# Kernel tuning notes

Measured on AMD Instinct MI355X. Metric: run time of the kernel, lower is better.

The kernel has to match this reference:

```python
import jax, jax.numpy as jnp
import numpy as np

R = 16                      # grid resolution per axis -> R**3 = 4096 experts
E = R ** 3
L_XYZ = 10                  # xyz positional-encoding frequencies -> input_ch = 63
L_DIR = 4                   # dir positional-encoding frequencies -> input_ch_views = 27
HID = 32                    # KiloNeRF W
AABB_MIN = -1.5
AABB_MAX = 1.5


def posenc(x, L):
    # NeRF positional encoding: [x, sin(2^l x), cos(2^l x)] for l in 0..L-1
    freqs = 2.0 ** jnp.arange(L, dtype=x.dtype)          # (L,)
    xb = x[..., None, :] * freqs[:, None]                # (..., L, 3)
    enc = jnp.concatenate([jnp.sin(xb), jnp.cos(xb)], axis=-1)  # (..., L, 6)
    return jnp.concatenate([x, enc.reshape(x.shape[:-1] + (-1,))], axis=-1)


def _linear_init(key, shape, fan_in):
    s = 1.0 / np.sqrt(fan_in)
    return jax.random.uniform(key, shape, jnp.float32, -s, s)


def setup_inputs() -> dict:
    key = jax.random.key(0)
    ks = jax.random.split(key, 16)
    in_pts = 3 + 6 * L_XYZ     # 63
    in_dirs = 3 + 6 * L_DIR    # 27
    in_view = in_dirs + HID    # 59
    return {
        "pts": jax.random.normal(ks[0], (1024, 64, 3), jnp.float32),
        "viewdirs": jax.random.normal(ks[1], (1024, 3), jnp.float32),
        "W1": _linear_init(ks[2], (E, in_pts, HID), in_pts),
        "b1": _linear_init(ks[3], (E, HID), in_pts),
        "W2": _linear_init(ks[4], (E, HID, HID), HID),
        "b2": _linear_init(ks[5], (E, HID), HID),
        "Wf": _linear_init(ks[6], (E, HID, HID), HID),
        "bf": _linear_init(ks[7], (E, HID), HID),
        "Wsig": _linear_init(ks[8], (E, HID, 1), HID),
        "bsig": _linear_init(ks[9], (E, 1), HID),
        "Wv": _linear_init(ks[10], (E, in_view, HID), in_view),
        "bv": _linear_init(ks[11], (E, HID), in_view),
        "Wrgb": _linear_init(ks[12], (E, HID, 3), HID),
        "brgb": _linear_init(ks[13], (E, 3), HID),
    }


def reference(pts, viewdirs, W1, b1, W2, b2, Wf, bf, Wsig, bsig, Wv, bv, Wrgb, brgb):
    N_rays, N_samples, _ = pts.shape
    p = pts.reshape(-1, 3)                                           # (N,3)
    d = jnp.broadcast_to(viewdirs[:, None, :], (N_rays, N_samples, 3)).reshape(-1, 3)

    # voxel index per point (Network._get_index)
    norm = (p - AABB_MIN) / (AABB_MAX - AABB_MIN)
    scaled = jnp.clip(norm * R, 0.0, R - 1.0)
    idx = scaled.astype(jnp.int32)                                   # (N,3)
    e = idx[:, 0] * (R * R) + idx[:, 1] * R + idx[:, 2]              # (N,) expert id

    xp = posenc(p, L_XYZ)                                            # (N,63)
    xd = posenc(d, L_DIR)                                            # (N,27)

    # grouped tiny-MLP dispatch, vectorized as per-point gathered weights
    h = jax.nn.relu(jnp.einsum('ni,nio->no', xp, W1[e]) + b1[e])     # (N,32)
    h = jax.nn.relu(jnp.einsum('ni,nio->no', h, W2[e]) + b2[e])      # (N,32)
    sigma = jnp.einsum('ni,nio->no', h, Wsig[e]) + bsig[e]           # (N,1)
    feat = jnp.einsum('ni,nio->no', h, Wf[e]) + bf[e]                # (N,32)
    hv = jnp.concatenate([feat, xd], axis=-1)                        # (N,59)
    hv = jax.nn.relu(jnp.einsum('ni,nio->no', hv, Wv[e]) + bv[e])    # (N,32)
    rgb = jnp.einsum('ni,nio->no', hv, Wrgb[e]) + brgb[e]            # (N,3)

    return rgb.reshape(N_rays, N_samples, 3), sigma.reshape(N_rays, N_samples, 1)
```

## Files before the change

### kernel.cpp

```cpp
#include <hip/hip_runtime.h>


#define CAP 256

#define WS_COUNTS 0
#define WS_OFFSETS 4096
#define WS_CURSOR 8192
#define WS_ORDER 12288

#define L_W1 0
#define L_W2 2016
#define L_WF 3040
#define L_WV 4064
#define L_WS 5952
#define L_WR 5984
#define L_B1 6080
#define L_B2 6112
#define L_BF 6144
#define L_BV 6176
#define L_BSR 6208
#define L_TOT 6212

__device__ __forceinline__ int expert_id(float px, float py, float pz) {
    float nx = (px - (-1.5f)) / 3.0f;
    float ny = (py - (-1.5f)) / 3.0f;
    float nz = (pz - (-1.5f)) / 3.0f;
    float sx = fminf(fmaxf(nx * 16.0f, 0.0f), 15.0f);
    float sy = fminf(fmaxf(ny * 16.0f, 0.0f), 15.0f);
    float sz = fminf(fmaxf(nz * 16.0f, 0.0f), 15.0f);
    return (int)sx * 256 + (int)sy * 16 + (int)sz;
}

__device__ __forceinline__ void gl16(const float* __restrict__ src, float* dst,
                                     int lane) {
    __builtin_amdgcn_global_load_lds(
        (const __attribute__((address_space(1))) unsigned int*)(src + 4 * lane),
        (__attribute__((address_space(3))) unsigned int*)(dst + 4 * lane),
        16, 0, 0);
}

__device__ __forceinline__ void stage_lds(const float* __restrict__ src,
                                          float* dst, int nfl, int lane) {
    int c = 0;
    for (; c + 256 <= nfl; c += 256) gl16(src + c, dst + c, lane);
    const int rem = nfl - c;
    if (4 * lane < rem) gl16(src + c, dst + c, lane);
}

__device__ __forceinline__ float enc_val(int idx, float x, float y, float z) {
    if (idx < 3) return (idx == 0) ? x : ((idx == 1) ? y : z);
    const int k = idx - 3;
    const int l = k / 6;
    const int r = k - 6 * l;
    const int c = (r < 3) ? r : r - 3;
    const float cv = (c == 0) ? x : ((c == 1) ? y : z);
    const float a = ldexpf(cv, l);
    return (r < 3) ? sinf(a) : cosf(a);
}

__global__ __launch_bounds__(256) void scatter_cap_kernel(
    const float* __restrict__ pts, int* __restrict__ counts,
    int* __restrict__ order, int n) {
    const int i = blockIdx.x * 256 + threadIdx.x;
    if (i < n) {
        const int e = expert_id(pts[3 * i + 0], pts[3 * i + 1], pts[3 * i + 2]);
        const int r = atomicAdd(&counts[e], 1);
        if (r < CAP) order[e * CAP + r] = i;
    }
}

__global__ __launch_bounds__(256) void hist_kernel(const float* __restrict__ pts,
                                                   int* __restrict__ counts, int n) {
    int i = blockIdx.x * 256 + threadIdx.x;
    if (i < n) {
        int e = expert_id(pts[3 * i + 0], pts[3 * i + 1], pts[3 * i + 2]);
        atomicAdd(&counts[e], 1);
    }
}

__global__ __launch_bounds__(256) void scan_kernel(const int* __restrict__ counts,
                                                   int* __restrict__ offsets,
                                                   int* __restrict__ cursor) {
    const int tid = threadIdx.x;
    const int lane = tid & 63, wave = tid >> 6;
    const int base = tid * 16;
    int c[16], loc[16], sum = 0;
#pragma unroll
    for (int j = 0; j < 16; ++j) c[j] = counts[base + j];
#pragma unroll
    for (int j = 0; j < 16; ++j) { loc[j] = sum; sum += c[j]; }
    int v = sum;
#pragma unroll
    for (int off = 1; off <= 32; off <<= 1) {
        int u = __shfl_up(v, off, 64);
        if (lane >= off) v += u;
    }
    __shared__ int wtot[4];
    if (lane == 63) wtot[wave] = v;
    __syncthreads();
    int wbase = 0;
    for (int w = 0; w < wave; ++w) wbase += wtot[w];
    const int excl = wbase + v - sum;
#pragma unroll
    for (int j = 0; j < 16; ++j) {
        int o = excl + loc[j];
        offsets[base + j] = o;
        cursor[base + j] = o;
    }
}

__global__ __launch_bounds__(256) void scatter_kernel(const float* __restrict__ pts,
                                                      int* __restrict__ cursor,
                                                      int* __restrict__ order, int n) {
    int i = blockIdx.x * 256 + threadIdx.x;
    if (i < n) {
        int e = expert_id(pts[3 * i + 0], pts[3 * i + 1], pts[3 * i + 2]);
        int pos = atomicAdd(&cursor[e], 1);
        order[pos] = i;
    }
}

__global__ __launch_bounds__(256) void expert_mlp_kernel(
    const float* __restrict__ pts, const float* __restrict__ viewdirs,
    const float* __restrict__ W1, const float* __restrict__ b1,
    const float* __restrict__ W2, const float* __restrict__ b2,
    const float* __restrict__ Wf, const float* __restrict__ bfc,
    const float* __restrict__ Wsig, const float* __restrict__ bsig,
    const float* __restrict__ Wv, const float* __restrict__ bv,
    const float* __restrict__ Wrgb, const float* __restrict__ brgb,
    const int* __restrict__ counts, const int* __restrict__ offsets,
    const int* __restrict__ order,
    float* __restrict__ out_rgb, float* __restrict__ out_sigma,
    int samples, int cap) {

    const int e = blockIdx.x;
    int cnt = counts[e];
    if (cnt == 0) return;
    if (cap > 0 && cnt > cap) cnt = cap;
    const int start = (cap > 0) ? e * cap : offsets[e];
    const int tid = threadIdx.x;
    const int wave = tid >> 6;
    const int lane = tid & 63;
    const int h = lane >> 5;
    const int o = lane & 31;

    __shared__ float lw[L_TOT];
    __shared__ float xs[4][8][64];
    __shared__ float xd[4][8][32];

    if (wave == 0) {
        stage_lds(W1 + (size_t)e * 2016, lw + L_W1, 2016, lane);
    } else if (wave == 1) {
        stage_lds(Wv + (size_t)e * 1888, lw + L_WV, 1888, lane);
    } else if (wave == 2) {
        stage_lds(W2 + (size_t)e * 1024, lw + L_W2, 1024, lane);
        stage_lds(Wsig + (size_t)e * 32, lw + L_WS, 32, lane);
        stage_lds(b1 + (size_t)e * 32, lw + L_B1, 32, lane);
        stage_lds(b2 + (size_t)e * 32, lw + L_B2, 32, lane);
    } else {
        stage_lds(Wf + (size_t)e * 1024, lw + L_WF, 1024, lane);
        stage_lds(Wrgb + (size_t)e * 96, lw + L_WR, 96, lane);
        stage_lds(bfc + (size_t)e * 32, lw + L_BF, 32, lane);
        stage_lds(bv + (size_t)e * 32, lw + L_BV, 32, lane);
    }
    if (tid == 0) lw[L_BSR] = bsig[e];
    if (tid < 3) lw[L_BSR + 1 + tid] = brgb[3 * e + tid];
    __syncthreads();

    const float b1o = lw[L_B1 + o];
    const float b2o = lw[L_B2 + o];
    const float bfo = lw[L_BF + o];
    const float bvo = lw[L_BV + o];
    const float wsg = lw[L_WS + o];
    const float wr0 = lw[L_WR + 3 * o + 0];
    const float wr1 = lw[L_WR + 3 * o + 1];
    const float wr2 = lw[L_WR + 3 * o + 2];
    const float bsg = lw[L_BSR];
    const float br0 = lw[L_BSR + 1], br1 = lw[L_BSR + 2], br2 = lw[L_BSR + 3];

    float* xsA = xs[wave][h];     float* xsB = xs[wave][2 + h];
    float* xsC = xs[wave][4 + h]; float* xsD = xs[wave][6 + h];
    float* xdA = xd[wave][h];     float* xdB = xd[wave][2 + h];
    float* xdC = xd[wave][4 + h]; float* xdD = xd[wave][6 + h];

    const bool pow2 = (samples & (samples - 1)) == 0;
    const int sh = 31 - __clz(samples);

    for (int s0 = 8 * wave; s0 < cnt; s0 += 32) {
        const int sA = s0 + h, sB = s0 + 2 + h, sC = s0 + 4 + h, sD = s0 + 6 + h;
        const bool lA = (sA < cnt), lB = (sB < cnt), lC = (sC < cnt), lD = (sD < cnt);
        const int ptA = order[start + (lA ? sA : cnt - 1)];
        const int ptB = order[start + (lB ? sB : cnt - 1)];
        const int ptC = order[start + (lC ? sC : cnt - 1)];
        const int ptD = order[start + (lD ? sD : cnt - 1)];

        const float pxA = pts[3 * ptA], pyA = pts[3 * ptA + 1], pzA = pts[3 * ptA + 2];
        const float pxB = pts[3 * ptB], pyB = pts[3 * ptB + 1], pzB = pts[3 * ptB + 2];
        const float pxC = pts[3 * ptC], pyC = pts[3 * ptC + 1], pzC = pts[3 * ptC + 2];
        const float pxD = pts[3 * ptD], pyD = pts[3 * ptD + 1], pzD = pts[3 * ptD + 2];
        const int rayA = pow2 ? (ptA >> sh) : (ptA / samples);
        const int rayB = pow2 ? (ptB >> sh) : (ptB / samples);
        const int rayC = pow2 ? (ptC >> sh) : (ptC / samples);
        const int rayD = pow2 ? (ptD >> sh) : (ptD / samples);
        const float dxA = viewdirs[3 * rayA], dyA = viewdirs[3 * rayA + 1], dzA = viewdirs[3 * rayA + 2];
        const float dxB = viewdirs[3 * rayB], dyB = viewdirs[3 * rayB + 1], dzB = viewdirs[3 * rayB + 2];
        const float dxC = viewdirs[3 * rayC], dyC = viewdirs[3 * rayC + 1], dzC = viewdirs[3 * rayC + 2];
        const float dxD = viewdirs[3 * rayD], dyD = viewdirs[3 * rayD + 1], dzD = viewdirs[3 * rayD + 2];

        xsA[o] = enc_val(o, pxA, pyA, pzA);
        xsB[o] = enc_val(o, pxB, pyB, pzB);
        xsC[o] = enc_val(o, pxC, pyC, pzC);
        xsD[o] = enc_val(o, pxD, pyD, pzD);
        if (o < 31) {
            xsA[o + 32] = enc_val(o + 32, pxA, pyA, pzA);
            xsB[o + 32] = enc_val(o + 32, pxB, pyB, pzB);
            xsC[o + 32] = enc_val(o + 32, pxC, pyC, pzC);
            xsD[o + 32] = enc_val(o + 32, pxD, pyD, pzD);
        }
        if (o < 27) {
            xdA[o] = enc_val(o, dxA, dyA, dzA);
            xdB[o] = enc_val(o, dxB, dyB, dzB);
            xdC[o] = enc_val(o, dxC, dyC, dzC);
            xdD[o] = enc_val(o, dxD, dyD, dzD);
        }

        float aA = b1o, aB = b1o, aC = b1o, aD = b1o;
#pragma unroll
        for (int q = 0; q < 15; ++q) {
            const float w0 = lw[L_W1 + (4 * q + 0) * 32 + o];
            const float w1 = lw[L_W1 + (4 * q + 1) * 32 + o];
            const float w2 = lw[L_W1 + (4 * q + 2) * 32 + o];
            const float w3 = lw[L_W1 + (4 * q + 3) * 32 + o];
            const float4 xA = *(const float4*)&xsA[4 * q];
            const float4 xB = *(const float4*)&xsB[4 * q];
            const float4 xC = *(const float4*)&xsC[4 * q];
            const float4 xD = *(const float4*)&xsD[4 * q];
            aA = fmaf(xA.x, w0, aA); aB = fmaf(xB.x, w0, aB);
            aC = fmaf(xC.x, w0, aC); aD = fmaf(xD.x, w0, aD);
            aA = fmaf(xA.y, w1, aA); aB = fmaf(xB.y, w1, aB);
            aC = fmaf(xC.y, w1, aC); aD = fmaf(xD.y, w1, aD);
            aA = fmaf(xA.z, w2, aA); aB = fmaf(xB.z, w2, aB);
            aC = fmaf(xC.z, w2, aC); aD = fmaf(xD.z, w2, aD);
            aA = fmaf(xA.w, w3, aA); aB = fmaf(xB.w, w3, aB);
            aC = fmaf(xC.w, w3, aC); aD = fmaf(xD.w, w3, aD);
        }
#pragma unroll
        for (int i = 60; i < 63; ++i) {
            const float w = lw[L_W1 + i * 32 + o];
            aA = fmaf(xsA[i], w, aA); aB = fmaf(xsB[i], w, aB);
            aC = fmaf(xsC[i], w, aC); aD = fmaf(xsD[i], w, aD);
        }
        xsA[o] = fmaxf(aA, 0.f);  xsB[o] = fmaxf(aB, 0.f);
        xsC[o] = fmaxf(aC, 0.f);  xsD[o] = fmaxf(aD, 0.f);

        aA = b2o; aB = b2o; aC = b2o; aD = b2o;
#pragma unroll
        for (int q = 0; q < 8; ++q) {
            const float w0 = lw[L_W2 + (4 * q + 0) * 32 + o];
            const float w1 = lw[L_W2 + (4 * q + 1) * 32 + o];
            const float w2 = lw[L_W2 + (4 * q + 2) * 32 + o];
            const float w3 = lw[L_W2 + (4 * q + 3) * 32 + o];
            const float4 xA = *(const float4*)&xsA[4 * q];
            const float4 xB = *(const float4*)&xsB[4 * q];
            const float4 xC = *(const float4*)&xsC[4 * q];
            const float4 xD = *(const float4*)&xsD[4 * q];
            aA = fmaf(xA.x, w0, aA); aB = fmaf(xB.x, w0, aB);
            aC = fmaf(xC.x, w0, aC); aD = fmaf(xD.x, w0, aD);
            aA = fmaf(xA.y, w1, aA); aB = fmaf(xB.y, w1, aB);
            aC = fmaf(xC.y, w1, aC); aD = fmaf(xD.y, w1, aD);
            aA = fmaf(xA.z, w2, aA); aB = fmaf(xB.z, w2, aB);
            aC = fmaf(xC.z, w2, aC); aD = fmaf(xD.z, w2, aD);
            aA = fmaf(xA.w, w3, aA); aB = fmaf(xB.w, w3, aB);
            aC = fmaf(xC.w, w3, aC); aD = fmaf(xD.w, w3, aD);
        }
        const float gA = fmaxf(aA, 0.f), gB = fmaxf(aB, 0.f);
        const float gC = fmaxf(aC, 0.f), gD = fmaxf(aD, 0.f);

        {
            float sA2 = gA * wsg, sB2 = gB * wsg, sC2 = gC * wsg, sD2 = gD * wsg;
#pragma unroll
            for (int m = 1; m <= 16; m <<= 1) {
                sA2 += __shfl_xor(sA2, m, 64);
                sB2 += __shfl_xor(sB2, m, 64);
                sC2 += __shfl_xor(sC2, m, 64);
                sD2 += __shfl_xor(sD2, m, 64);
            }
            if (o == 0) {
                if (lA) out_sigma[ptA] = sA2 + bsg;
                if (lB) out_sigma[ptB] = sB2 + bsg;
                if (lC) out_sigma[ptC] = sC2 + bsg;
                if (lD) out_sigma[ptD] = sD2 + bsg;
            }
        }
        xsA[o] = gA; xsB[o] = gB; xsC[o] = gC; xsD[o] = gD;

        aA = bfo; aB = bfo; aC = bfo; aD = bfo;
#pragma unroll
        for (int q = 0; q < 8; ++q) {
            const float w0 = lw[L_WF + (4 * q + 0) * 32 + o];
            const float w1 = lw[L_WF + (4 * q + 1) * 32 + o];
            const float w2 = lw[L_WF + (4 * q + 2) * 32 + o];
            const float w3 = lw[L_WF + (4 * q + 3) * 32 + o];
            const float4 xA = *(const float4*)&xsA[4 * q];
            const float4 xB = *(const float4*)&xsB[4 * q];
            const float4 xC = *(const float4*)&xsC[4 * q];
            const float4 xD = *(const float4*)&xsD[4 * q];
            aA = fmaf(xA.x, w0, aA); aB = fmaf(xB.x, w0, aB);
            aC = fmaf(xC.x, w0, aC); aD = fmaf(xD.x, w0, aD);
            aA = fmaf(xA.y, w1, aA); aB = fmaf(xB.y, w1, aB);
            aC = fmaf(xC.y, w1, aC); aD = fmaf(xD.y, w1, aD);
            aA = fmaf(xA.z, w2, aA); aB = fmaf(xB.z, w2, aB);
            aC = fmaf(xC.z, w2, aC); aD = fmaf(xD.z, w2, aD);
            aA = fmaf(xA.w, w3, aA); aB = fmaf(xB.w, w3, aB);
            aC = fmaf(xC.w, w3, aC); aD = fmaf(xD.w, w3, aD);
        }
        xsA[o] = aA; xsB[o] = aB; xsC[o] = aC; xsD[o] = aD;

        float vA = bvo, vB = bvo, vC = bvo, vD = bvo;
#pragma unroll
        for (int q = 0; q < 8; ++q) {
            const float w0 = lw[L_WV + (4 * q + 0) * 32 + o];
            const float w1 = lw[L_WV + (4 * q + 1) * 32 + o];
            const float w2 = lw[L_WV + (4 * q + 2) * 32 + o];
            const float w3 = lw[L_WV + (4 * q + 3) * 32 + o];
            const float4 xA = *(const float4*)&xsA[4 * q];
            const float4 xB = *(const float4*)&xsB[4 * q];
            const float4 xC = *(const float4*)&xsC[4 * q];
            const float4 xD = *(const float4*)&xsD[4 * q];
            vA = fmaf(xA.x, w0, vA); vB = fmaf(xB.x, w0, vB);
            vC = fmaf(xC.x, w0, vC); vD = fmaf(xD.x, w0, vD);
            vA = fmaf(xA.y, w1, vA); vB = fmaf(xB.y, w1, vB);
            vC = fmaf(xC.y, w1, vC); vD = fmaf(xD.y, w1, vD);
            vA = fmaf(xA.z, w2, vA); vB = fmaf(xB.z, w2, vB);
            vC = fmaf(xC.z, w2, vC); vD = fmaf(xD.z, w2, vD);
            vA = fmaf(xA.w, w3, vA); vB = fmaf(xB.w, w3, vB);
            vC = fmaf(xC.w, w3, vC); vD = fmaf(xD.w, w3, vD);
        }
#pragma unroll
        for (int q = 0; q < 6; ++q) {
            const float w0 = lw[L_WV + (32 + 4 * q + 0) * 32 + o];
            const float w1 = lw[L_WV + (32 + 4 * q + 1) * 32 + o];
            const float w2 = lw[L_WV + (32 + 4 * q + 2) * 32 + o];
            const float w3 = lw[L_WV + (32 + 4 * q + 3) * 32 + o];
            const float4 xA = *(const float4*)&xdA[4 * q];
            const float4 xB = *(const float4*)&xdB[4 * q];
            const float4 xC = *(const float4*)&xdC[4 * q];
            const float4 xD = *(const float4*)&xdD[4 * q];
            vA = fmaf(xA.x, w0, vA); vB = fmaf(xB.x, w0, vB);
            vC = fmaf(xC.x, w0, vC); vD = fmaf(xD.x, w0, vD);
            vA = fmaf(xA.y, w1, vA); vB = fmaf(xB.y, w1, vB);
            vC = fmaf(xC.y, w1, vC); vD = fmaf(xD.y, w1, vD);
            vA = fmaf(xA.z, w2, vA); vB = fmaf(xB.z, w2, vB);
            vC = fmaf(xC.z, w2, vC); vD = fmaf(xD.z, w2, vD);
            vA = fmaf(xA.w, w3, vA); vB = fmaf(xB.w, w3, vB);
            vC = fmaf(xC.w, w3, vC); vD = fmaf(xD.w, w3, vD);
        }
#pragma unroll
        for (int i = 24; i < 27; ++i) {
            const float w = lw[L_WV + (32 + i) * 32 + o];
            vA = fmaf(xdA[i], w, vA); vB = fmaf(xdB[i], w, vB);
            vC = fmaf(xdC[i], w, vC); vD = fmaf(xdD[i], w, vD);
        }
        const float hA = fmaxf(vA, 0.f), hB = fmaxf(vB, 0.f);
        const float hC = fmaxf(vC, 0.f), hD = fmaxf(vD, 0.f);

        {
            float r0A = hA * wr0, r1A = hA * wr1, r2A = hA * wr2;
            float r0B = hB * wr0, r1B = hB * wr1, r2B = hB * wr2;
            float r0C = hC * wr0, r1C = hC * wr1, r2C = hC * wr2;
            float r0D = hD * wr0, r1D = hD * wr1, r2D = hD * wr2;
#pragma unroll
            for (int m = 1; m <= 16; m <<= 1) {
                r0A += __shfl_xor(r0A, m, 64); r1A += __shfl_xor(r1A, m, 64); r2A += __shfl_xor(r2A, m, 64);
                r0B += __shfl_xor(r0B, m, 64); r1B += __shfl_xor(r1B, m, 64); r2B += __shfl_xor(r2B, m, 64);
                r0C += __shfl_xor(r0C, m, 64); r1C += __shfl_xor(r1C, m, 64); r2C += __shfl_xor(r2C, m, 64);
                r0D += __shfl_xor(r0D, m, 64); r1D += __shfl_xor(r1D, m, 64); r2D += __shfl_xor(r2D, m, 64);
            }
            if (o == 0) {
                if (lA) { out_rgb[3 * ptA] = r0A + br0; out_rgb[3 * ptA + 1] = r1A + br1; out_rgb[3 * ptA + 2] = r2A + br2; }
                if (lB) { out_rgb[3 * ptB] = r0B + br0; out_rgb[3 * ptB + 1] = r1B + br1; out_rgb[3 * ptB + 2] = r2B + br2; }
                if (lC) { out_rgb[3 * ptC] = r0C + br0; out_rgb[3 * ptC + 1] = r1C + br1; out_rgb[3 * ptC + 2] = r2C + br2; }
                if (lD) { out_rgb[3 * ptD] = r0D + br0; out_rgb[3 * ptD + 1] = r1D + br1; out_rgb[3 * ptD + 2] = r2D + br2; }
            }
        }
    }
}

extern "C" void kernel_launch(void* const* d_in, const int* in_sizes, int n_in,
                              void* d_out, int out_size, void* d_ws, size_t ws_size,
                              hipStream_t stream) {
    const float* pts      = (const float*)d_in[0];
    const float* viewdirs = (const float*)d_in[1];
    const float* W1   = (const float*)d_in[2];
    const float* b1   = (const float*)d_in[3];
    const float* W2   = (const float*)d_in[4];
    const float* b2   = (const float*)d_in[5];
    const float* Wf   = (const float*)d_in[6];
    const float* bfc  = (const float*)d_in[7];
    const float* Wsig = (const float*)d_in[8];
    const float* bsig = (const float*)d_in[9];
    const float* Wv   = (const float*)d_in[10];
    const float* bv   = (const float*)d_in[11];
    const float* Wrgb = (const float*)d_in[12];
    const float* brgb = (const float*)d_in[13];

    const int n = in_sizes[0] / 3;
    const int n_rays = in_sizes[1] / 3;
    const int samples = n / n_rays;

    float* out_rgb = (float*)d_out;
    float* out_sigma = out_rgb + (size_t)n * 3;

    int* ws = (int*)d_ws;
    int* counts = ws + WS_COUNTS;
    int* offsets = ws + WS_OFFSETS;
    int* cursor = ws + WS_CURSOR;
    int* order = ws + WS_ORDER;

    const size_t need_cap = ((size_t)WS_ORDER + (size_t)4096 * CAP) * sizeof(int);
    if (ws_size >= need_cap) {
        hipMemsetAsync(counts, 0, 4096 * sizeof(int), stream);
        scatter_cap_kernel<<<(n + 255) / 256, 256, 0, stream>>>(pts, counts, order, n);
        expert_mlp_kernel<<<4096, 256, 0, stream>>>(
            pts, viewdirs, W1, b1, W2, b2, Wf, bfc, Wsig, bsig, Wv, bv, Wrgb, brgb,
            counts, offsets, order, out_rgb, out_sigma, samples, CAP);
    } else {
        hipMemsetAsync(counts, 0, 4096 * sizeof(int), stream);
        hist_kernel<<<(n + 255) / 256, 256, 0, stream>>>(pts, counts, n);
        scan_kernel<<<1, 256, 0, stream>>>(counts, offsets, cursor);
        scatter_kernel<<<(n + 255) / 256, 256, 0, stream>>>(pts, cursor, order, n);
        expert_mlp_kernel<<<4096, 256, 0, stream>>>(
            pts, viewdirs, W1, b1, W2, b2, Wf, bfc, Wsig, bsig, Wv, bv, Wrgb, brgb,
            counts, offsets, order, out_rgb, out_sigma, samples, 0);
    }
}
```

Before: 210.5 us.

## Process four experts per block with a dedicated producer wave double-buffering weights

Each block now handles up to four consecutive non-empty experts instead of one. A fifth wave acts as a producer that stages the next expert's weight slab into a second LDS buffer while the four compute waves work on the current expert. The goal is to hide weight-load latency and cut per-block launch and setup overhead. In exchange, the grid is four times smaller, LDS use roughly doubles (which may reduce occupancy), and a single wave now does all the staging with block-wide syncs between experts.

```diff
diff --git a/kernel.cpp b/kernel.cpp
--- a/kernel.cpp
+++ b/kernel.cpp
@@ -19,7 +19,7 @@
 #define L_BF 6144
 #define L_BV 6176
 #define L_BSR 6208
-#define L_TOT 6212
+#define SLABF 6224
 
 __device__ __forceinline__ int expert_id(float px, float py, float pz) {
     float nx = (px - (-1.5f)) / 3.0f;
@@ -45,6 +45,28 @@
     for (; c + 256 <= nfl; c += 256) gl16(src + c, dst + c, lane);
     const int rem = nfl - c;
     if (4 * lane < rem) gl16(src + c, dst + c, lane);
+}
+
+__device__ __forceinline__ void stage_slab(
+    float* dst, int e, int lane,
+    const float* __restrict__ W1, const float* __restrict__ W2,
+    const float* __restrict__ Wf, const float* __restrict__ Wv,
+    const float* __restrict__ Wsig, const float* __restrict__ Wrgb,
+    const float* __restrict__ b1, const float* __restrict__ b2,
+    const float* __restrict__ bfc, const float* __restrict__ bv,
+    const float* __restrict__ bsig, const float* __restrict__ brgb) {
+    stage_lds(W1 + (size_t)e * 2016, dst + L_W1, 2016, lane);
+    stage_lds(Wv + (size_t)e * 1888, dst + L_WV, 1888, lane);
+    stage_lds(W2 + (size_t)e * 1024, dst + L_W2, 1024, lane);
+    stage_lds(Wf + (size_t)e * 1024, dst + L_WF, 1024, lane);
+    stage_lds(Wsig + (size_t)e * 32, dst + L_WS, 32, lane);
+    stage_lds(Wrgb + (size_t)e * 96, dst + L_WR, 96, lane);
+    stage_lds(b1 + (size_t)e * 32, dst + L_B1, 32, lane);
+    stage_lds(b2 + (size_t)e * 32, dst + L_B2, 32, lane);
+    stage_lds(bfc + (size_t)e * 32, dst + L_BF, 32, lane);
+    stage_lds(bv + (size_t)e * 32, dst + L_BV, 32, lane);
+    if (lane == 0) dst[L_BSR] = bsig[e];
+    if (lane < 3) dst[L_BSR + 1 + lane] = brgb[3 * e + lane];
 }
 
 __device__ __forceinline__ float enc_val(int idx, float x, float y, float z) {
@@ -120,7 +142,7 @@
     }
 }
 
-__global__ __launch_bounds__(256) void expert_mlp_kernel(
+__global__ __launch_bounds__(320) void expert_mlp_kernel(
     const float* __restrict__ pts, const float* __restrict__ viewdirs,
     const float* __restrict__ W1, const float* __restrict__ b1,
     const float* __restrict__ W2, const float* __restrict__ b2,
@@ -133,256 +155,265 @@
     float* __restrict__ out_rgb, float* __restrict__ out_sigma,
     int samples, int cap) {
 
-    const int e = blockIdx.x;
-    int cnt = counts[e];
-    if (cnt == 0) return;
-    if (cap > 0 && cnt > cap) cnt = cap;
-    const int start = (cap > 0) ? e * cap : offsets[e];
     const int tid = threadIdx.x;
-    const int wave = tid >> 6;
+    const int wv = tid >> 6;
     const int lane = tid & 63;
-    const int h = lane >> 5;
-    const int o = lane & 31;
-
-    __shared__ float lw[L_TOT];
+
+    unsigned pack = 0;
+    int K = 0;
+#pragma unroll
+    for (int j = 0; j < 4; ++j) {
+        if (counts[4 * blockIdx.x + j] > 0) { pack |= (unsigned)j << (8 * K); ++K; }
+    }
+    if (K == 0) return;
+
+    __shared__ float lw[2 * SLABF];
     __shared__ float xs[4][8][64];
     __shared__ float xd[4][8][32];
 
-    if (wave == 0) {
-        stage_lds(W1 + (size_t)e * 2016, lw + L_W1, 2016, lane);
-    } else if (wave == 1) {
-        stage_lds(Wv + (size_t)e * 1888, lw + L_WV, 1888, lane);
-    } else if (wave == 2) {
-        stage_lds(W2 + (size_t)e * 1024, lw + L_W2, 1024, lane);
-        stage_lds(Wsig + (size_t)e * 32, lw + L_WS, 32, lane);
-        stage_lds(b1 + (size_t)e * 32, lw + L_B1, 32, lane);
-        stage_lds(b2 + (size_t)e * 32, lw + L_B2, 32, lane);
-    } else {
-        stage_lds(Wf + (size_t)e * 1024, lw + L_WF, 1024, lane);
-        stage_lds(Wrgb + (size_t)e * 96, lw + L_WR, 96, lane);
-        stage_lds(bfc + (size_t)e * 32, lw + L_BF, 32, lane);
-        stage_lds(bv + (size_t)e * 32, lw + L_BV, 32, lane);
-    }
-    if (tid == 0) lw[L_BSR] = bsig[e];
-    if (tid < 3) lw[L_BSR + 1 + tid] = brgb[3 * e + tid];
-    __syncthreads();
-
-    const float b1o = lw[L_B1 + o];
-    const float b2o = lw[L_B2 + o];
-    const float bfo = lw[L_BF + o];
-    const float bvo = lw[L_BV + o];
-    const float wsg = lw[L_WS + o];
-    const float wr0 = lw[L_WR + 3 * o + 0];
-    const float wr1 = lw[L_WR + 3 * o + 1];
-    const float wr2 = lw[L_WR + 3 * o + 2];
-    const float bsg = lw[L_BSR];
-    const float br0 = lw[L_BSR + 1], br1 = lw[L_BSR + 2], br2 = lw[L_BSR + 3];
-
-    float* xsA = xs[wave][h];     float* xsB = xs[wave][2 + h];
-    float* xsC = xs[wave][4 + h]; float* xsD = xs[wave][6 + h];
-    float* xdA = xd[wave][h];     float* xdB = xd[wave][2 + h];
-    float* xdC = xd[wave][4 + h]; float* xdD = xd[wave][6 + h];
-
     const bool pow2 = (samples & (samples - 1)) == 0;
     const int sh = 31 - __clz(samples);
 
-    for (int s0 = 8 * wave; s0 < cnt; s0 += 32) {
-        const int sA = s0 + h, sB = s0 + 2 + h, sC = s0 + 4 + h, sD = s0 + 6 + h;
-        const bool lA = (sA < cnt), lB = (sB < cnt), lC = (sC < cnt), lD = (sD < cnt);
-        const int ptA = order[start + (lA ? sA : cnt - 1)];
-        const int ptB = order[start + (lB ? sB : cnt - 1)];
-        const int ptC = order[start + (lC ? sC : cnt - 1)];
-        const int ptD = order[start + (lD ? sD : cnt - 1)];
-
-        const float pxA = pts[3 * ptA], pyA = pts[3 * ptA + 1], pzA = pts[3 * ptA + 2];
-        const float pxB = pts[3 * ptB], pyB = pts[3 * ptB + 1], pzB = pts[3 * ptB + 2];
-        const float pxC = pts[3 * ptC], pyC = pts[3 * ptC + 1], pzC = pts[3 * ptC + 2];
-        const float pxD = pts[3 * ptD], pyD = pts[3 * ptD + 1], pzD = pts[3 * ptD + 2];
-        const int rayA = pow2 ? (ptA >> sh) : (ptA / samples);
-        const int rayB = pow2 ? (ptB >> sh) : (ptB / samples);
-        const int rayC = pow2 ? (ptC >> sh) : (ptC / samples);
-        const int rayD = pow2 ? (ptD >> sh) : (ptD / samples);
-        const float dxA = viewdirs[3 * rayA], dyA = viewdirs[3 * rayA + 1], dzA = viewdirs[3 * rayA + 2];
-        const float dxB = viewdirs[3 * rayB], dyB = viewdirs[3 * rayB + 1], dzB = viewdirs[3 * rayB + 2];
-        const float dxC = viewdirs[3 * rayC], dyC = viewdirs[3 * rayC + 1], dzC = viewdirs[3 * rayC + 2];
-        const float dxD = viewdirs[3 * rayD], dyD = viewdirs[3 * rayD + 1], dzD = viewdirs[3 * rayD + 2];
-
-        xsA[o] = enc_val(o, pxA, pyA, pzA);
-        xsB[o] = enc_val(o, pxB, pyB, pzB);
-        xsC[o] = enc_val(o, pxC, pyC, pzC);
-        xsD[o] = enc_val(o, pxD, pyD, pzD);
-        if (o < 31) {
-            xsA[o + 32] = enc_val(o + 32, pxA, pyA, pzA);
-            xsB[o + 32] = enc_val(o + 32, pxB, pyB, pzB);
-            xsC[o + 32] = enc_val(o + 32, pxC, pyC, pzC);
-            xsD[o + 32] = enc_val(o + 32, pxD, pyD, pzD);
-        }
-        if (o < 27) {
-            xdA[o] = enc_val(o, dxA, dyA, dzA);
-            xdB[o] = enc_val(o, dxB, dyB, dzB);
-            xdC[o] = enc_val(o, dxC, dyC, dzC);
-            xdD[o] = enc_val(o, dxD, dyD, dzD);
-        }
-
-        float aA = b1o, aB = b1o, aC = b1o, aD = b1o;
-#pragma unroll
-        for (int q = 0; q < 15; ++q) {
-            const float w0 = lw[L_W1 + (4 * q + 0) * 32 + o];
-            const float w1 = lw[L_W1 + (4 * q + 1) * 32 + o];
-            const float w2 = lw[L_W1 + (4 * q + 2) * 32 + o];
-            const float w3 = lw[L_W1 + (4 * q + 3) * 32 + o];
-            const float4 xA = *(const float4*)&xsA[4 * q];
-            const float4 xB = *(const float4*)&xsB[4 * q];
-            const float4 xC = *(const float4*)&xsC[4 * q];
-            const float4 xD = *(const float4*)&xsD[4 * q];
-            aA = fmaf(xA.x, w0, aA); aB = fmaf(xB.x, w0, aB);
-            aC = fmaf(xC.x, w0, aC); aD = fmaf(xD.x, w0, aD);
-            aA = fmaf(xA.y, w1, aA); aB = fmaf(xB.y, w1, aB);
-            aC = fmaf(xC.y, w1, aC); aD = fmaf(xD.y, w1, aD);
-            aA = fmaf(xA.z, w2, aA); aB = fmaf(xB.z, w2, aB);
-            aC = fmaf(xC.z, w2, aC); aD = fmaf(xD.z, w2, aD);
-            aA = fmaf(xA.w, w3, aA); aB = fmaf(xB.w, w3, aB);
-            aC = fmaf(xC.w, w3, aC); aD = fmaf(xD.w, w3, aD);
-        }
-#pragma unroll
-        for (int i = 60; i < 63; ++i) {
-            const float w = lw[L_W1 + i * 32 + o];
-            aA = fmaf(xsA[i], w, aA); aB = fmaf(xsB[i], w, aB);
-            aC = fmaf(xsC[i], w, aC); aD = fmaf(xsD[i], w, aD);
-        }
-        xsA[o] = fmaxf(aA, 0.f);  xsB[o] = fmaxf(aB, 0.f);
-        xsC[o] = fmaxf(aC, 0.f);  xsD[o] = fmaxf(aD, 0.f);
-
-        aA = b2o; aB = b2o; aC = b2o; aD = b2o;
-#pragma unroll
-        for (int q = 0; q < 8; ++q) {
-            const float w0 = lw[L_W2 + (4 * q + 0) * 32 + o];
-            const float w1 = lw[L_W2 + (4 * q + 1) * 32 + o];
-            const float w2 = lw[L_W2 + (4 * q + 2) * 32 + o];
-            const float w3 = lw[L_W2 + (4 * q + 3) * 32 + o];
-            const float4 xA = *(const float4*)&xsA[4 * q];
-            const float4 xB = *(const float4*)&xsB[4 * q];
-            const float4 xC = *(const float4*)&xsC[4 * q];
-            const float4 xD = *(const float4*)&xsD[4 * q];
-            aA = fmaf(xA.x, w0, aA); aB = fmaf(xB.x, w0, aB);
-            aC = fmaf(xC.x, w0, aC); aD = fmaf(xD.x, w0, aD);
-            aA = fmaf(xA.y, w1, aA); aB = fmaf(xB.y, w1, aB);
-            aC = fmaf(xC.y, w1, aC); aD = fmaf(xD.y, w1, aD);
-            aA = fmaf(xA.z, w2, aA); aB = fmaf(xB.z, w2, aB);
-            aC = fmaf(xC.z, w2, aC); aD = fmaf(xD.z, w2, aD);
-            aA = fmaf(xA.w, w3, aA); aB = fmaf(xB.w, w3, aB);
-            aC = fmaf(xC.w, w3, aC); aD = fmaf(xD.w, w3, aD);
-        }
-        const float gA = fmaxf(aA, 0.f), gB = fmaxf(aB, 0.f);
-        const float gC = fmaxf(aC, 0.f), gD = fmaxf(aD, 0.f);
-
-        {
-            float sA2 = gA * wsg, sB2 = gB * wsg, sC2 = gC * wsg, sD2 = gD * wsg;
-#pragma unroll
-            for (int m = 1; m <= 16; m <<= 1) {
-                sA2 += __shfl_xor(sA2, m, 64);
-                sB2 += __shfl_xor(sB2, m, 64);
-                sC2 += __shfl_xor(sC2, m, 64);
-                sD2 += __shfl_xor(sD2, m, 64);
+    if (wv == 4) {
+        const int e0 = 4 * blockIdx.x + (int)(pack & 3u);
+        stage_slab(lw, e0, lane, W1, W2, Wf, Wv, Wsig, Wrgb, b1, b2, bfc, bv,
+                   bsig, brgb);
+    }
+    __syncthreads();
+
+    for (int k = 0; k < K; ++k) {
+        float* lwc = lw + (k & 1) * SLABF;
+        if (wv == 4) {
+            if (k + 1 < K) {
+                const int en = 4 * blockIdx.x + (int)((pack >> (8 * (k + 1))) & 3u);
+                stage_slab(lw + ((k + 1) & 1) * SLABF, en, lane, W1, W2, Wf, Wv,
+                           Wsig, Wrgb, b1, b2, bfc, bv, bsig, brgb);
             }
-            if (o == 0) {
-                if (lA) out_sigma[ptA] = sA2 + bsg;
-                if (lB) out_sigma[ptB] = sB2 + bsg;
-                if (lC) out_sigma[ptC] = sC2 + bsg;
-                if (lD) out_sigma[ptD] = sD2 + bsg;
+        } else {
+            const int e = 4 * blockIdx.x + (int)((pack >> (8 * k)) & 3u);
+            int cnt = counts[e];
+            if (cap > 0 && cnt > cap) cnt = cap;
+            const int start = (cap > 0) ? e * cap : offsets[e];
+            const int wave = wv;
+            const int h = lane >> 5;
+            const int o = lane & 31;
+
+            const float b1o = lwc[L_B1 + o];
+            const float b2o = lwc[L_B2 + o];
+            const float bfo = lwc[L_BF + o];
+            const float bvo = lwc[L_BV + o];
+            const float wsg = lwc[L_WS + o];
+            const float wr0 = lwc[L_WR + 3 * o + 0];
+            const float wr1 = lwc[L_WR + 3 * o + 1];
+            const float wr2 = lwc[L_WR + 3 * o + 2];
+            const float bsg = lwc[L_BSR];
+            const float br0 = lwc[L_BSR + 1], br1 = lwc[L_BSR + 2], br2 = lwc[L_BSR + 3];
+
+            float* xsA = xs[wave][h];     float* xsB = xs[wave][2 + h];
+            float* xsC = xs[wave][4 + h]; float* xsD = xs[wave][6 + h];
+            float* xdA = xd[wave][h];     float* xdB = xd[wave][2 + h];
+            float* xdC = xd[wave][4 + h]; float* xdD = xd[wave][6 + h];
+
+            for (int s0 = 8 * wave; s0 < cnt; s0 += 32) {
+                const int sA = s0 + h, sB = s0 + 2 + h, sC = s0 + 4 + h, sD = s0 + 6 + h;
+                const bool lA = (sA < cnt), lB = (sB < cnt), lC = (sC < cnt), lD = (sD < cnt);
+                const int ptA = order[start + (lA ? sA : cnt - 1)];
+                const int ptB = order[start + (lB ? sB : cnt - 1)];
+                const int ptC = order[start + (lC ? sC : cnt - 1)];
+                const int ptD = order[start + (lD ? sD : cnt - 1)];
+
+                const float pxA = pts[3 * ptA], pyA = pts[3 * ptA + 1], pzA = pts[3 * ptA + 2];
+                const float pxB = pts[3 * ptB], pyB = pts[3 * ptB + 1], pzB = pts[3 * ptB + 2];
+                const float pxC = pts[3 * ptC], pyC = pts[3 * ptC + 1], pzC = pts[3 * ptC + 2];
+                const float pxD = pts[3 * ptD], pyD = pts[3 * ptD + 1], pzD = pts[3 * ptD + 2];
+                const int rayA = pow2 ? (ptA >> sh) : (ptA / samples);
+                const int rayB = pow2 ? (ptB >> sh) : (ptB / samples);
+                const int rayC = pow2 ? (ptC >> sh) : (ptC / samples);
+                const int rayD = pow2 ? (ptD >> sh) : (ptD / samples);
+                const float dxA = viewdirs[3 * rayA], dyA = viewdirs[3 * rayA + 1], dzA = viewdirs[3 * rayA + 2];
+                const float dxB = viewdirs[3 * rayB], dyB = viewdirs[3 * rayB + 1], dzB = viewdirs[3 * rayB + 2];
+                const float dxC = viewdirs[3 * rayC], dyC = viewdirs[3 * rayC + 1], dzC = viewdirs[3 * rayC + 2];
+                const float dxD = viewdirs[3 * rayD], dyD = viewdirs[3 * rayD + 1], dzD = viewdirs[3 * rayD + 2];
+
+                xsA[o] = enc_val(o, pxA, pyA, pzA);
+                xsB[o] = enc_val(o, pxB, pyB, pzB);
+                xsC[o] = enc_val(o, pxC, pyC, pzC);
+                xsD[o] = enc_val(o, pxD, pyD, pzD);
+                if (o < 31) {
+                    xsA[o + 32] = enc_val(o + 32, pxA, pyA, pzA);
+                    xsB[o + 32] = enc_val(o + 32, pxB, pyB, pzB);
+                    xsC[o + 32] = enc_val(o + 32, pxC, pyC, pzC);
+                    xsD[o + 32] = enc_val(o + 32, pxD, pyD, pzD);
+                }
+                if (o < 27) {
+                    xdA[o] = enc_val(o, dxA, dyA, dzA);
+                    xdB[o] = enc_val(o, dxB, dyB, dzB);
+                    xdC[o] = enc_val(o, dxC, dyC, dzC);
+                    xdD[o] = enc_val(o, dxD, dyD, dzD);
+                }
+
+                float aA = b1o, aB = b1o, aC = b1o, aD = b1o;
+#pragma unroll
+                for (int q = 0; q < 15; ++q) {
+                    const float w0 = lwc[L_W1 + (4 * q + 0) * 32 + o];
+                    const float w1 = lwc[L_W1 + (4 * q + 1) * 32 + o];
+                    const float w2 = lwc[L_W1 + (4 * q + 2) * 32 + o];
+                    const float w3 = lwc[L_W1 + (4 * q + 3) * 32 + o];
+                    const float4 xA = *(const float4*)&xsA[4 * q];
+                    const float4 xB = *(const float4*)&xsB[4 * q];
+                    const float4 xC = *(const float4*)&xsC[4 * q];
+                    const float4 xD = *(const float4*)&xsD[4 * q];
+                    aA = fmaf(xA.x, w0, aA); aB = fmaf(xB.x, w0, aB);
+                    aC = fmaf(xC.x, w0, aC); aD = fmaf(xD.x, w0, aD);
+                    aA = fmaf(xA.y, w1, aA); aB = fmaf(xB.y, w1, aB);
+                    aC = fmaf(xC.y, w1, aC); aD = fmaf(xD.y, w1, aD);
+                    aA = fmaf(xA.z, w2, aA); aB = fmaf(xB.z, w2, aB);
+                    aC = fmaf(xC.z, w2, aC); aD = fmaf(xD.z, w2, aD);
+                    aA = fmaf(xA.w, w3, aA); aB = fmaf(xB.w, w3, aB);
+                    aC = fmaf(xC.w, w3, aC); aD = fmaf(xD.w, w3, aD);
+                }
+#pragma unroll
+                for (int i = 60; i < 63; ++i) {
+                    const float w = lwc[L_W1 + i * 32 + o];
+                    aA = fmaf(xsA[i], w, aA); aB = fmaf(xsB[i], w, aB);
+                    aC = fmaf(xsC[i], w, aC); aD = fmaf(xsD[i], w, aD);
+                }
+                xsA[o] = fmaxf(aA, 0.f);  xsB[o] = fmaxf(aB, 0.f);
+                xsC[o] = fmaxf(aC, 0.f);  xsD[o] = fmaxf(aD, 0.f);
+
+                aA = b2o; aB = b2o; aC = b2o; aD = b2o;
+#pragma unroll
+                for (int q = 0; q < 8; ++q) {
+                    const float w0 = lwc[L_W2 + (4 * q + 0) * 32 + o];
+                    const float w1 = lwc[L_W2 + (4 * q + 1) * 32 + o];
+                    const float w2 = lwc[L_W2 + (4 * q + 2) * 32 + o];
+                    const float w3 = lwc[L_W2 + (4 * q + 3) * 32 + o];
+                    const float4 xA = *(const float4*)&xsA[4 * q];
+                    const float4 xB = *(const float4*)&xsB[4 * q];
+                    const float4 xC = *(const float4*)&xsC[4 * q];
+                    const float4 xD = *(const float4*)&xsD[4 * q];
+                    aA = fmaf(xA.x, w0, aA); aB = fmaf(xB.x, w0, aB);
+                    aC = fmaf(xC.x, w0, aC); aD = fmaf(xD.x, w0, aD);
+                    aA = fmaf(xA.y, w1, aA); aB = fmaf(xB.y, w1, aB);
+                    aC = fmaf(xC.y, w1, aC); aD = fmaf(xD.y, w1, aD);
+                    aA = fmaf(xA.z, w2, aA); aB = fmaf(xB.z, w2, aB);
+                    aC = fmaf(xC.z, w2, aC); aD = fmaf(xD.z, w2, aD);
+                    aA = fmaf(xA.w, w3, aA); aB = fmaf(xB.w, w3, aB);
+                    aC = fmaf(xC.w, w3, aC); aD = fmaf(xD.w, w3, aD);
+                }
+                const float gA = fmaxf(aA, 0.f), gB = fmaxf(aB, 0.f);
+                const float gC = fmaxf(aC, 0.f), gD = fmaxf(aD, 0.f);
+
+                {
+                    float sA2 = gA * wsg, sB2 = gB * wsg, sC2 = gC * wsg, sD2 = gD * wsg;
+#pragma unroll
+                    for (int m = 1; m <= 16; m <<= 1) {
+                        sA2 += __shfl_xor(sA2, m, 64);
+                        sB2 += __shfl_xor(sB2, m, 64);
+                        sC2 += __shfl_xor(sC2, m, 64);
+                        sD2 += __shfl_xor(sD2, m, 64);
+                    }
+                    if (o == 0) {
+                        if (lA) out_sigma[ptA] = sA2 + bsg;
+                        if (lB) out_sigma[ptB] = sB2 + bsg;
+                        if (lC) out_sigma[ptC] = sC2 + bsg;
+                        if (lD) out_sigma[ptD] = sD2 + bsg;
+                    }
+                }
+                xsA[o] = gA; xsB[o] = gB; xsC[o] = gC; xsD[o] = gD;
+
+                aA = bfo; aB = bfo; aC = bfo; aD = bfo;
+#pragma unroll
+                for (int q = 0; q < 8; ++q) {
+                    const float w0 = lwc[L_WF + (4 * q + 0) * 32 + o];
+                    const float w1 = lwc[L_WF + (4 * q + 1) * 32 + o];
+                    const float w2 = lwc[L_WF + (4 * q + 2) * 32 + o];
+                    const float w3 = lwc[L_WF + (4 * q + 3) * 32 + o];
+                    const float4 xA = *(const float4*)&xsA[4 * q];
+                    const float4 xB = *(const float4*)&xsB[4 * q];
+                    const float4 xC = *(const float4*)&xsC[4 * q];
+                    const float4 xD = *(const float4*)&xsD[4 * q];
+                    aA = fmaf(xA.x, w0, aA); aB = fmaf(xB.x, w0, aB);
+                    aC = fmaf(xC.x, w0, aC); aD = fmaf(xD.x, w0, aD);
+                    aA = fmaf(xA.y, w1, aA); aB = fmaf(xB.y, w1, aB);
+                    aC = fmaf(xC.y, w1, aC); aD = fmaf(xD.y, w1, aD);
+                    aA = fmaf(xA.z, w2, aA); aB = fmaf(xB.z, w2, aB);
+                    aC = fmaf(xC.z, w2, aC); aD = fmaf(xD.z, w2, aD);
+                    aA = fmaf(xA.w, w3, aA); aB = fmaf(xB.w, w3, aB);
+                    aC = fmaf(xC.w, w3, aC); aD = fmaf(xD.w, w3, aD);
+                }
+                xsA[o] = aA; xsB[o] = aB; xsC[o] = aC; xsD[o] = aD;
+
+                float vA = bvo, vB = bvo, vC = bvo, vD = bvo;
+#pragma unroll
+                for (int q = 0; q < 8; ++q) {
+                    const float w0 = lwc[L_WV + (4 * q + 0) * 32 + o];
+                    const float w1 = lwc[L_WV + (4 * q + 1) * 32 + o];
+                    const float w2 = lwc[L_WV + (4 * q + 2) * 32 + o];
+                    const float w3 = lwc[L_WV + (4 * q + 3) * 32 + o];
+                    const float4 xA = *(const float4*)&xsA[4 * q];
+                    const float4 xB = *(const float4*)&xsB[4 * q];
+                    const float4 xC = *(const float4*)&xsC[4 * q];
+                    const float4 xD = *(const float4*)&xsD[4 * q];
+                    vA = fmaf(xA.x, w0, vA); vB = fmaf(xB.x, w0, vB);
+                    vC = fmaf(xC.x, w0, vC); vD = fmaf(xD.x, w0, vD);
+                    vA = fmaf(xA.y, w1, vA); vB = fmaf(xB.y, w1, vB);
+                    vC = fmaf(xC.y, w1, vC); vD = fmaf(xD.y, w1, vD);
+                    vA = fmaf(xA.z, w2, vA); vB = fmaf(xB.z, w2, vB);
+                    vC = fmaf(xC.z, w2, vC); vD = fmaf(xD.z, w2, vD);
+                    vA = fmaf(xA.w, w3, vA); vB = fmaf(xB.w, w3, vB);
+                    vC = fmaf(xC.w, w3, vC); vD = fmaf(xD.w, w3, vD);
+                }
+#pragma unroll
+                for (int q = 0; q < 6; ++q) {
+                    const float w0 = lwc[L_WV + (32 + 4 * q + 0) * 32 + o];
+                    const float w1 = lwc[L_WV + (32 + 4 * q + 1) * 32 + o];
+                    const float w2 = lwc[L_WV + (32 + 4 * q + 2) * 32 + o];
+                    const float w3 = lwc[L_WV + (32 + 4 * q + 3) * 32 + o];
+                    const float4 xA = *(const float4*)&xdA[4 * q];
+                    const float4 xB = *(const float4*)&xdB[4 * q];
+                    const float4 xC = *(const float4*)&xdC[4 * q];
+                    const float4 xD = *(const float4*)&xdD[4 * q];
+                    vA = fmaf(xA.x, w0, vA); vB = fmaf(xB.x, w0, vB);
+                    vC = fmaf(xC.x, w0, vC); vD = fmaf(xD.x, w0, vD);
+                    vA = fmaf(xA.y, w1, vA); vB = fmaf(xB.y, w1, vB);
+                    vC = fmaf(xC.y, w1, vC); vD = fmaf(xD.y, w1, vD);
+                    vA = fmaf(xA.z, w2, vA); vB = fmaf(xB.z, w2, vB);
+                    vC = fmaf(xC.z, w2, vC); vD = fmaf(xD.z, w2, vD);
+                    vA = fmaf(xA.w, w3, vA); vB = fmaf(xB.w, w3, vB);
+                    vC = fmaf(xC.w, w3, vC); vD = fmaf(xD.w, w3, vD);
+                }
+#pragma unroll
+                for (int i = 24; i < 27; ++i) {
+                    const float w = lwc[L_WV + (32 + i) * 32 + o];
+                    vA = fmaf(xdA[i], w, vA); vB = fmaf(xdB[i], w, vB);
+                    vC = fmaf(xdC[i], w, vC); vD = fmaf(xdD[i], w, vD);
+                }
+                const float hA = fmaxf(vA, 0.f), hB = fmaxf(vB, 0.f);
+                const float hC = fmaxf(vC, 0.f), hD = fmaxf(vD, 0.f);
+
+                {
+                    float r0A = hA * wr0, r1A = hA * wr1, r2A = hA * wr2;
+                    float r0B = hB * wr0, r1B = hB * wr1, r2B = hB * wr2;
+                    float r0C = hC * wr0, r1C = hC * wr1, r2C = hC * wr2;
+                    float r0D = hD * wr0, r1D = hD * wr1, r2D = hD * wr2;
+#pragma unroll
+                    for (int m = 1; m <= 16; m <<= 1) {
+                        r0A += __shfl_xor(r0A, m, 64); r1A += __shfl_xor(r1A, m, 64); r2A += __shfl_xor(r2A, m, 64);
+                        r0B += __shfl_xor(r0B, m, 64); r1B += __shfl_xor(r1B, m, 64); r2B += __shfl_xor(r2B, m, 64);
+                        r0C += __shfl_xor(r0C, m, 64); r1C += __shfl_xor(r1C, m, 64); r2C += __shfl_xor(r2C, m, 64);
+                        r0D += __shfl_xor(r0D, m, 64); r1D += __shfl_xor(r1D, m, 64); r2D += __shfl_xor(r2D, m, 64);
+                    }
+                    if (o == 0) {
+                        if (lA) { out_rgb[3 * ptA] = r0A + br0; out_rgb[3 * ptA + 1] = r1A + br1; out_rgb[3 * ptA + 2] = r2A + br2; }
+                        if (lB) { out_rgb[3 * ptB] = r0B + br0; out_rgb[3 * ptB + 1] = r1B + br1; out_rgb[3 * ptB + 2] = r2B + br2; }
+                        if (lC) { out_rgb[3 * ptC] = r0C + br0; out_rgb[3 * ptC + 1] = r1C + br1; out_rgb[3 * ptC + 2] = r2C + br2; }
+                        if (lD) { out_rgb[3 * ptD] = r0D + br0; out_rgb[3 * ptD + 1] = r1D + br1; out_rgb[3 * ptD + 2] = r2D + br2; }
+                    }
+                }
             }
         }
-        xsA[o] = gA; xsB[o] = gB; xsC[o] = gC; xsD[o] = gD;
-
-        aA = bfo; aB = bfo; aC = bfo; aD = bfo;
-#pragma unroll
-        for (int q = 0; q < 8; ++q) {
-            const float w0 = lw[L_WF + (4 * q + 0) * 32 + o];
-            const float w1 = lw[L_WF + (4 * q + 1) * 32 + o];
-            const float w2 = lw[L_WF + (4 * q + 2) * 32 + o];
-            const float w3 = lw[L_WF + (4 * q + 3) * 32 + o];
-            const float4 xA = *(const float4*)&xsA[4 * q];
-            const float4 xB = *(const float4*)&xsB[4 * q];
-            const float4 xC = *(const float4*)&xsC[4 * q];
-            const float4 xD = *(const float4*)&xsD[4 * q];
-            aA = fmaf(xA.x, w0, aA); aB = fmaf(xB.x, w0, aB);
-            aC = fmaf(xC.x, w0, aC); aD = fmaf(xD.x, w0, aD);
-            aA = fmaf(xA.y, w1, aA); aB = fmaf(xB.y, w1, aB);
-            aC = fmaf(xC.y, w1, aC); aD = fmaf(xD.y, w1, aD);
-            aA = fmaf(xA.z, w2, aA); aB = fmaf(xB.z, w2, aB);
-            aC = fmaf(xC.z, w2, aC); aD = fmaf(xD.z, w2, aD);
-            aA = fmaf(xA.w, w3, aA); aB = fmaf(xB.w, w3, aB);
-            aC = fmaf(xC.w, w3, aC); aD = fmaf(xD.w, w3, aD);
-        }
-        xsA[o] = aA; xsB[o] = aB; xsC[o] = aC; xsD[o] = aD;
-
-        float vA = bvo, vB = bvo, vC = bvo, vD = bvo;
-#pragma unroll
-        for (int q = 0; q < 8; ++q) {
-            const float w0 = lw[L_WV + (4 * q + 0) * 32 + o];
-            const float w1 = lw[L_WV + (4 * q + 1) * 32 + o];
-            const float w2 = lw[L_WV + (4 * q + 2) * 32 + o];
-            const float w3 = lw[L_WV + (4 * q + 3) * 32 + o];
-            const float4 xA = *(const float4*)&xsA[4 * q];
-            const float4 xB = *(const float4*)&xsB[4 * q];
-            const float4 xC = *(const float4*)&xsC[4 * q];
-            const float4 xD = *(const float4*)&xsD[4 * q];
-            vA = fmaf(xA.x, w0, vA); vB = fmaf(xB.x, w0, vB);
-            vC = fmaf(xC.x, w0, vC); vD = fmaf(xD.x, w0, vD);
-            vA = fmaf(xA.y, w1, vA); vB = fmaf(xB.y, w1, vB);
-            vC = fmaf(xC.y, w1, vC); vD = fmaf(xD.y, w1, vD);
-            vA = fmaf(xA.z, w2, vA); vB = fmaf(xB.z, w2, vB);
-            vC = fmaf(xC.z, w2, vC); vD = fmaf(xD.z, w2, vD);
-            vA = fmaf(xA.w, w3, vA); vB = fmaf(xB.w, w3, vB);
-            vC = fmaf(xC.w, w3, vC); vD = fmaf(xD.w, w3, vD);
-        }
-#pragma unroll
-        for (int q = 0; q < 6; ++q) {
-            const float w0 = lw[L_WV + (32 + 4 * q + 0) * 32 + o];
-            const float w1 = lw[L_WV + (32 + 4 * q + 1) * 32 + o];
-            const float w2 = lw[L_WV + (32 + 4 * q + 2) * 32 + o];
-            const float w3 = lw[L_WV + (32 + 4 * q + 3) * 32 + o];
-            const float4 xA = *(const float4*)&xdA[4 * q];
-            const float4 xB = *(const float4*)&xdB[4 * q];
-            const float4 xC = *(const float4*)&xdC[4 * q];
-            const float4 xD = *(const float4*)&xdD[4 * q];
-            vA = fmaf(xA.x, w0, vA); vB = fmaf(xB.x, w0, vB);
-            vC = fmaf(xC.x, w0, vC); vD = fmaf(xD.x, w0, vD);
-            vA = fmaf(xA.y, w1, vA); vB = fmaf(xB.y, w1, vB);
-            vC = fmaf(xC.y, w1, vC); vD = fmaf(xD.y, w1, vD);
-            vA = fmaf(xA.z, w2, vA); vB = fmaf(xB.z, w2, vB);
-            vC = fmaf(xC.z, w2, vC); vD = fmaf(xD.z, w2, vD);
-            vA = fmaf(xA.w, w3, vA); vB = fmaf(xB.w, w3, vB);
-            vC = fmaf(xC.w, w3, vC); vD = fmaf(xD.w, w3, vD);
-        }
-#pragma unroll
-        for (int i = 24; i < 27; ++i) {
-            const float w = lw[L_WV + (32 + i) * 32 + o];
-            vA = fmaf(xdA[i], w, vA); vB = fmaf(xdB[i], w, vB);
-            vC = fmaf(xdC[i], w, vC); vD = fmaf(xdD[i], w, vD);
-        }
-        const float hA = fmaxf(vA, 0.f), hB = fmaxf(vB, 0.f);
-        const float hC = fmaxf(vC, 0.f), hD = fmaxf(vD, 0.f);
-
-        {
-            float r0A = hA * wr0, r1A = hA * wr1, r2A = hA * wr2;
-            float r0B = hB * wr0, r1B = hB * wr1, r2B = hB * wr2;
-            float r0C = hC * wr0, r1C = hC * wr1, r2C = hC * wr2;
-            float r0D = hD * wr0, r1D = hD * wr1, r2D = hD * wr2;
-#pragma unroll
-            for (int m = 1; m <= 16; m <<= 1) {
-                r0A += __shfl_xor(r0A, m, 64); r1A += __shfl_xor(r1A, m, 64); r2A += __shfl_xor(r2A, m, 64);
-                r0B += __shfl_xor(r0B, m, 64); r1B += __shfl_xor(r1B, m, 64); r2B += __shfl_xor(r2B, m, 64);
-                r0C += __shfl_xor(r0C, m, 64); r1C += __shfl_xor(r1C, m, 64); r2C += __shfl_xor(r2C, m, 64);
-                r0D += __shfl_xor(r0D, m, 64); r1D += __shfl_xor(r1D, m, 64); r2D += __shfl_xor(r2D, m, 64);
-            }
-            if (o == 0) {
-                if (lA) { out_rgb[3 * ptA] = r0A + br0; out_rgb[3 * ptA + 1] = r1A + br1; out_rgb[3 * ptA + 2] = r2A + br2; }
-                if (lB) { out_rgb[3 * ptB] = r0B + br0; out_rgb[3 * ptB + 1] = r1B + br1; out_rgb[3 * ptB + 2] = r2B + br2; }
-                if (lC) { out_rgb[3 * ptC] = r0C + br0; out_rgb[3 * ptC + 1] = r1C + br1; out_rgb[3 * ptC + 2] = r2C + br2; }
-                if (lD) { out_rgb[3 * ptD] = r0D + br0; out_rgb[3 * ptD + 1] = r1D + br1; out_rgb[3 * ptD + 2] = r2D + br2; }
-            }
-        }
+        __syncthreads();
     }
 }
 
@@ -421,7 +452,7 @@
     if (ws_size >= need_cap) {
         hipMemsetAsync(counts, 0, 4096 * sizeof(int), stream);
         scatter_cap_kernel<<<(n + 255) / 256, 256, 0, stream>>>(pts, counts, order, n);
-        expert_mlp_kernel<<<4096, 256, 0, stream>>>(
+        expert_mlp_kernel<<<1024, 320, 0, stream>>>(
             pts, viewdirs, W1, b1, W2, b2, Wf, bfc, Wsig, bsig, Wv, bv, Wrgb, brgb,
             counts, offsets, order, out_rgb, out_sigma, samples, CAP);
     } else {
@@ -429,7 +460,7 @@
         hist_kernel<<<(n + 255) / 256, 256, 0, stream>>>(pts, counts, n);
         scan_kernel<<<1, 256, 0, stream>>>(counts, offsets, cursor);
         scatter_kernel<<<(n + 255) / 256, 256, 0, stream>>>(pts, cursor, order, n);
-        expert_mlp_kernel<<<4096, 256, 0, stream>>>(
+        expert_mlp_kernel<<<1024, 320, 0, stream>>>(
             pts, viewdirs, W1, b1, W2, b2, Wf, bfc, Wsig, bsig, Wv, bv, Wrgb, brgb,
             counts, offsets, order, out_rgb, out_sigma, samples, 0);
     }
```

After: 318.8 us. 1.51x slower.
